# Kernel optimization log

Measured on AMD Instinct MI355X. Metric: run time of the kernel, lower is better.

## Reference

```python
import jax, jax.numpy as jnp
import numpy as np

E = 384          # embed_dim
NH = 12          # num_heads
HD = E // NH     # head_dim = 32
NC = 16          # num_clusters
SCALE = HD ** -0.5


def setup_inputs() -> dict:
    key = jax.random.key(0)
    ks = jax.random.split(key, 6)
    b, h, w = 8, 64, 64
    x = jax.random.normal(ks[0], (b, E, h, w), jnp.float32)
    qkv_w = jax.random.normal(ks[1], (3 * E, E), jnp.float32) * 0.02
    qkv_b = jnp.zeros((3 * E,), jnp.float32)
    lepe_w = jax.random.normal(ks[2], (E, 1, 5, 5), jnp.float32) * 0.02
    lepe_b = jnp.zeros((E,), jnp.float32)
    out_w = jax.random.normal(ks[3], (E, E), jnp.float32) * 0.02
    out_b = jnp.zeros((E,), jnp.float32)
    return dict(x=x, qkv_w=qkv_w, qkv_b=qkv_b, lepe_w=lepe_w,
                lepe_b=lepe_b, out_w=out_w, out_b=out_b)


def _gather_tokens(t, idx):
    # t: (b, n, l, d), idx: (b, n, l)
    return jnp.take_along_axis(t, idx[..., None], axis=2)


def reference(x, qkv_w, qkv_b, lepe_w, lepe_b, out_w, out_b):
    b, _, h, w = x.shape
    l = h * w
    lc = l // NC  # tokens per cluster

    # 1x1 conv qkv projection (channel order: [q heads | k heads | v heads])
    qkv = jnp.einsum('bchw,oc->bohw', x, qkv_w) + qkv_b[None, :, None, None]

    # lepe: 5x5 depthwise conv on the v channel slice
    v_img = qkv[:, 2 * E:]
    lepe = jax.lax.conv_general_dilated(
        v_img, lepe_w, (1, 1), ((2, 2), (2, 2)),
        feature_group_count=E,
        dimension_numbers=('NCHW', 'OIHW', 'NCHW')) + lepe_b[None, :, None, None]

    # 'b (m n d) h w -> m b n (h w) d'
    qkv = qkv.reshape(b, 3, NH, HD, l).transpose(1, 0, 2, 4, 3)  # (3,b,n,l,d)
    q, k, v = qkv[0], qkv[1], qkv[2]
    k = k * SCALE

    # cosine-similarity sort routing (sort_sim(k, k))
    cls = jnp.mean(k, axis=2, keepdims=True)                       # (b,n,1,d)
    cls = cls / jnp.maximum(jnp.linalg.norm(cls, axis=-1, keepdims=True), 1e-12)
    kn = k / jnp.maximum(jnp.linalg.norm(k, axis=-1, keepdims=True), 1e-12)
    cos = jnp.einsum('bnod,bnld->bnl', cls, kn)                    # (b,n,l)
    idx = jnp.argsort(cos, axis=-1)                                # (b,n,l)

    qs = _gather_tokens(q, idx).reshape(b, NH, NC, lc, HD)
    ks_ = _gather_tokens(k, idx).reshape(b, NH, NC, lc, HD)
    vs = _gather_tokens(v, idx).reshape(b, NH, NC, lc, HD)

    # blockwise (per-cluster) attention
    attn = jax.nn.softmax(jnp.einsum('bncld,bncmd->bnclm', qs, ks_), axis=-1)
    o = jnp.einsum('bnclm,bncmd->bncld', attn, vs).reshape(b, NH, l, HD)

    # restore original token order (inverse permutation)
    inv = jnp.argsort(idx, axis=-1)
    o = _gather_tokens(o, inv)

    # 'b n (h w) d -> b (n d) h w'
    o = o.transpose(0, 1, 3, 2).reshape(b, E, h, w)

    res = o + lepe
    return jnp.einsum('bchw,oc->bohw', res, out_w) + out_b[None, :, None, None]
```

## Files before the change

kernel.cpp:

```cpp
#include <hip/hip_runtime.h>
#include <math.h>

#define SCALE_F   0.17677669529663687f
#define SCALE_L2E 0.25505837072959003f

using bf16x8 = __attribute__((ext_vector_type(8))) __bf16;
using f32x2  = __attribute__((ext_vector_type(2))) float;
using f32x4  = __attribute__((ext_vector_type(4))) float;
using f32x16 = __attribute__((ext_vector_type(16))) float;
using uint2e = __attribute__((ext_vector_type(2))) unsigned int;

__device__ inline unsigned short f2bf(float x) {
    __bf16 h = (__bf16)x;
    return __builtin_bit_cast(unsigned short, h);
}
__device__ inline float bf2f(unsigned short u) {
    unsigned int x = ((unsigned int)u) << 16;
    return __builtin_bit_cast(float, x);
}
__device__ inline unsigned int packbf(float a, float b) {
    return (unsigned int)f2bf(a) | ((unsigned int)f2bf(b) << 16);
}
__device__ inline bf16x8 ldfrag(const unsigned short* p) {
    return __builtin_bit_cast(bf16x8, *reinterpret_cast<const uint4*>(p));
}

__global__ __launch_bounds__(512)
void gemm_k_kernel(const float* __restrict__ A, const float* __restrict__ Bmat,
                   const float* __restrict__ bias, float* __restrict__ CT)
{
    const int bm = blockIdx.x, bn = blockIdx.y, bz = blockIdx.z;
    const float* Bp = Bmat + (long)bz * 384 * 4096;
    float* Cp = CT + (long)bz * 4096 * 384;
    __shared__ float As[32][132];
    __shared__ float BsF[32 * 136];
    const int tid = threadIdx.x;
    const int tx = tid & 15, ty = tid >> 4;
    const int m0 = bm * 128, n0 = bn * 128;

    const int sr0 = tid >> 5,          sq0 = tid & 31;
    const int sr1 = (tid + 512) >> 5,  sq1 = (tid + 512) & 31;
    const int wB0 = sr0 * 136 + ((sq0 & 1) << 6) + ((sq0 >> 1) << 2);
    const int wB1 = sr1 * 136 + ((sq1 & 1) << 6) + ((sq1 >> 1) << 2);

    f32x2 acc2[4][4];
    #pragma unroll
    for (int i = 0; i < 4; ++i)
        #pragma unroll
        for (int p = 0; p < 4; ++p) acc2[i][p] = (f32x2){0.f, 0.f};

    float4 bPf0 = *reinterpret_cast<const float4*>(&Bp[(long)sr0 * 4096 + n0 + sq0 * 4]);
    float4 bPf1 = *reinterpret_cast<const float4*>(&Bp[(long)sr1 * 4096 + n0 + sq1 * 4]);

    for (int k0 = 0; k0 < 384; k0 += 32) {
        if (k0) __syncthreads();
        *reinterpret_cast<float4*>(&BsF[wB0]) = bPf0;
        *reinterpret_cast<float4*>(&BsF[wB1]) = bPf1;
        #pragma unroll
        for (int it = 0; it < 2; ++it) {
            int slot = tid + it * 512;
            int rA = slot >> 3, cA = slot & 7;
            float4 av = *reinterpret_cast<const float4*>(&A[(long)(384 + m0 + rA) * 384 + k0 + cA * 4]);
            As[cA * 4 + 0][rA] = av.x; As[cA * 4 + 1][rA] = av.y;
            As[cA * 4 + 2][rA] = av.z; As[cA * 4 + 3][rA] = av.w;
        }
        __syncthreads();
        if (k0 + 32 < 384) {
            bPf0 = *reinterpret_cast<const float4*>(&Bp[(long)(k0 + 32 + sr0) * 4096 + n0 + sq0 * 4]);
            bPf1 = *reinterpret_cast<const float4*>(&Bp[(long)(k0 + 32 + sr1) * 4096 + n0 + sq1 * 4]);
        }
        #pragma unroll
        for (int kk = 0; kk < 32; ++kk) {
            float a[4];
            *reinterpret_cast<float4*>(&a[0]) = *reinterpret_cast<const float4*>(&As[kk][ty * 4]);
            float4 blo = *reinterpret_cast<const float4*>(&BsF[kk * 136 + tx * 4]);
            float4 bhi = *reinterpret_cast<const float4*>(&BsF[kk * 136 + 64 + tx * 4]);
            f32x2 b2[4];
            b2[0] = (f32x2){blo.x, blo.y}; b2[1] = (f32x2){blo.z, blo.w};
            b2[2] = (f32x2){bhi.x, bhi.y}; b2[3] = (f32x2){bhi.z, bhi.w};
            #pragma unroll
            for (int i = 0; i < 4; ++i) {
                f32x2 a2 = (f32x2){a[i], a[i]};
                #pragma unroll
                for (int p = 0; p < 4; ++p)
                    acc2[i][p] = __builtin_elementwise_fma(a2, b2[p], acc2[i][p]);
            }
        }
    }

    float bv[4];
    #pragma unroll
    for (int i = 0; i < 4; ++i) bv[i] = bias[384 + m0 + ty * 4 + i];
    #pragma unroll
    for (int p = 0; p < 4; ++p)
        #pragma unroll
        for (int c = 0; c < 2; ++c) {
            int j = 2 * p + c;
            long tok = n0 + tx * 8 + j;
            float4 v = make_float4(acc2[0][p][c] + bv[0], acc2[1][p][c] + bv[1],
                                   acc2[2][p][c] + bv[2], acc2[3][p][c] + bv[3]);
            *reinterpret_cast<float4*>(Cp + tok * 384 + m0 + ty * 4) = v;
        }
}

template<bool SPLIT, int SM>
__global__ __launch_bounds__(256)
void mfma_nt_kernel(const unsigned short* __restrict__ Ah, const unsigned short* __restrict__ Al,
                    const unsigned short* __restrict__ Bh, const unsigned short* __restrict__ Bl,
                    const float* __restrict__ bias, void* __restrict__ Cout,
                    int K, int lda, int ldb,
                    long strideAb, long strideBb, long strideCb)
{
    extern __shared__ unsigned short smem[];
    unsigned short* As  = smem;
    unsigned short* Bs  = smem + 5120;
    unsigned short* Asl = smem + 10240;
    unsigned short* Bsl = smem + 15360;
    const int bm = blockIdx.x, bn = blockIdx.y, bz = blockIdx.z;
    const unsigned short* Ap = Ah + (long)bz * strideAb;
    const unsigned short* Bp = Bh + (long)bz * strideBb;
    const unsigned short* Alp = nullptr;
    const unsigned short* Blp = nullptr;
    if constexpr (SPLIT) {
        Alp = Al + (long)bz * strideAb;
        Blp = Bl + (long)bz * strideBb;
    }
    const int tid = threadIdx.x;
    const int lane = tid & 63, wid = tid >> 6;
    const int wr = wid >> 1, wc = wid & 1;
    const int l15 = lane & 15, l4 = lane >> 4;
    const int m0 = bm * 128, n0 = bn * 128;

    const f32x4 Z4 = {0.f, 0.f, 0.f, 0.f};
    f32x4 acc[4][4];
    #pragma unroll
    for (int i = 0; i < 4; ++i)
        #pragma unroll
        for (int j = 0; j < 4; ++j) acc[i][j] = Z4;

    for (int k0 = 0; k0 < K; k0 += 32) {
        if (k0) __syncthreads();
        #pragma unroll
        for (int it = 0; it < 2; ++it) {
            int slot = tid + it * 256;
            int r = slot >> 2, cq = slot & 3;
            *reinterpret_cast<uint4*>(&As[r * 40 + cq * 8]) =
                *reinterpret_cast<const uint4*>(&Ap[(long)(m0 + r) * lda + k0 + cq * 8]);
            *reinterpret_cast<uint4*>(&Bs[r * 40 + cq * 8]) =
                *reinterpret_cast<const uint4*>(&Bp[(long)(n0 + r) * ldb + k0 + cq * 8]);
            if constexpr (SPLIT) {
                *reinterpret_cast<uint4*>(&Asl[r * 40 + cq * 8]) =
                    *reinterpret_cast<const uint4*>(&Alp[(long)(m0 + r) * lda + k0 + cq * 8]);
                *reinterpret_cast<uint4*>(&Bsl[r * 40 + cq * 8]) =
                    *reinterpret_cast<const uint4*>(&Blp[(long)(n0 + r) * ldb + k0 + cq * 8]);
            }
        }
        __syncthreads();

        bf16x8 af[4], bg[4], afl[4], bgl[4];
        #pragma unroll
        for (int f = 0; f < 4; ++f) {
            af[f] = ldfrag(&As[(wr * 64 + f * 16 + l15) * 40 + l4 * 8]);
            bg[f] = ldfrag(&Bs[(wc * 64 + f * 16 + l15) * 40 + l4 * 8]);
        }
        if constexpr (SPLIT) {
            #pragma unroll
            for (int f = 0; f < 4; ++f) {
                afl[f] = ldfrag(&Asl[(wr * 64 + f * 16 + l15) * 40 + l4 * 8]);
                bgl[f] = ldfrag(&Bsl[(wc * 64 + f * 16 + l15) * 40 + l4 * 8]);
            }
        }
        #pragma unroll
        for (int fi = 0; fi < 4; ++fi)
            #pragma unroll
            for (int fj = 0; fj < 4; ++fj) {
                acc[fi][fj] = __builtin_amdgcn_mfma_f32_16x16x32_bf16(af[fi], bg[fj], acc[fi][fj], 0, 0, 0);
                if constexpr (SPLIT) {
                    acc[fi][fj] = __builtin_amdgcn_mfma_f32_16x16x32_bf16(af[fi], bgl[fj], acc[fi][fj], 0, 0, 0);
                    acc[fi][fj] = __builtin_amdgcn_mfma_f32_16x16x32_bf16(afl[fi], bg[fj], acc[fi][fj], 0, 0, 0);
                }
            }
    }

    if constexpr (SM == 0) {
        unsigned short* Cq = (unsigned short*)Cout + (long)bz * strideCb;
        #pragma unroll
        for (int fi = 0; fi < 4; ++fi)
            #pragma unroll
            for (int fj = 0; fj < 4; ++fj) {
                const int m = m0 + wr * 64 + fi * 16 + l4 * 4;
                const int t = n0 + wc * 64 + fj * 16 + l15;
                ushort4 h;
                h.x = f2bf(acc[fi][fj][0] + bias[m + 0]);
                h.y = f2bf(acc[fi][fj][1] + bias[m + 1]);
                h.z = f2bf(acc[fi][fj][2] + bias[m + 2]);
                h.w = f2bf(acc[fi][fj][3] + bias[m + 3]);
                *reinterpret_cast<ushort4*>(&Cq[(long)t * 768 + m]) = h;
            }
    } else {
        float* Cf = (float*)Cout + (long)bz * strideCb;
        #pragma unroll
        for (int fi = 0; fi < 4; ++fi)
            #pragma unroll
            for (int fj = 0; fj < 4; ++fj) {
                const int t = m0 + wr * 64 + fi * 16 + l4 * 4;
                const int m = n0 + wc * 64 + fj * 16 + l15;
                const float bv = bias[m];
                float4 v = make_float4(acc[fi][fj][0] + bv, acc[fi][fj][1] + bv,
                                       acc[fi][fj][2] + bv, acc[fi][fj][3] + bv);
                *reinterpret_cast<float4*>(&Cf[(long)m * 4096 + t]) = v;
            }
    }
}

__global__ __launch_bounds__(256)
void convert_w_kernel(const float* __restrict__ qkv_w, const float* __restrict__ qkv_b,
                      const float* __restrict__ out_w,
                      unsigned short* __restrict__ Wqv, float* __restrict__ qvb,
                      unsigned short* __restrict__ owh, unsigned short* __restrict__ owl)
{
    const int total = 294912 + 147456 + 768;
    for (int i = blockIdx.x * 256 + threadIdx.x; i < total; i += gridDim.x * 256) {
        if (i < 294912) {
            int m = i / 384, k = i - m * 384;
            int src = (m < 384) ? m : m + 384;
            Wqv[i] = f2bf(qkv_w[(long)src * 384 + k]);
        } else if (i < 294912 + 147456) {
            int o = i - 294912;
            float w = out_w[o];
            unsigned short h = f2bf(w);
            owh[o] = h;
            owl[o] = f2bf(w - bf2f(h));
        } else {
            int m = i - 294912 - 147456;
            qvb[m] = qkv_b[(m < 384) ? m : m + 384];
        }
    }
}

__global__ __launch_bounds__(256)
void transpose_x_kernel(const float* __restrict__ x, unsigned short* __restrict__ xbT)
{
    const int t0 = blockIdx.x * 64, c0 = blockIdx.y * 64, b = blockIdx.z;
    __shared__ float tl[64][65];
    const int tid = threadIdx.x;
    #pragma unroll
    for (int i = 0; i < 16; ++i) {
        int cr = (tid >> 6) + i * 4, tc = tid & 63;
        tl[cr][tc] = x[((long)b * 384 + c0 + cr) * 4096 + t0 + tc];
    }
    __syncthreads();
    #pragma unroll
    for (int i = 0; i < 8; ++i) {
        int tr = (tid >> 5) + i * 8, c2 = (tid & 31) * 2;
        unsigned int u = packbf(tl[c2][tr], tl[c2 + 1][tr]);
        *reinterpret_cast<unsigned int*>(&xbT[((long)b * 4096 + t0 + tr) * 384 + c0 + c2]) = u;
    }
}

__global__ __launch_bounds__(256)
void cls_kernel(const float* __restrict__ Kf32, float* __restrict__ clsg)
{
    const int bn = blockIdx.x;
    const int b = bn / 12, n = bn % 12;
    const float* kb = Kf32 + (long)b * 4096 * 384 + n * 32;
    __shared__ float part[256][33];
    const int tid = threadIdx.x;
    float acc[32];
    #pragma unroll
    for (int d = 0; d < 32; ++d) acc[d] = 0.f;
    for (int i = 0; i < 16; ++i) {
        long tok = tid + i * 256;
        const float* kr = kb + tok * 384;
        #pragma unroll
        for (int d = 0; d < 32; ++d) acc[d] += kr[d];
    }
    #pragma unroll
    for (int d = 0; d < 32; ++d) part[tid][d] = acc[d];
    __syncthreads();
    if (tid < 32) {
        double s = 0.0;
        for (int t = 0; t < 256; ++t) s += (double)part[t][tid];
        part[0][tid] = (float)s;
    }
    __syncthreads();
    if (tid == 0) {
        double nn = 0.0;
        for (int d = 0; d < 32; ++d) { double v = (double)part[0][d]; nn += v * v; }
        double inv = 1.0 / sqrt(nn > 1e-300 ? nn : 1e-300);
        for (int d = 0; d < 32; ++d) clsg[bn * 32 + d] = (float)((double)part[0][d] * inv);
    }
}

__global__ __launch_bounds__(256)
void cos_lepe_kernel(const float* __restrict__ Kf32, const float* __restrict__ clsg,
                     float* __restrict__ cosv,
                     const unsigned short* __restrict__ qvB, const float* __restrict__ w5,
                     const float* __restrict__ wb, unsigned short* __restrict__ lepeT)
{
    __shared__ float tile[12 * 68 * 16];
    const int bid = blockIdx.x;
    const int tid = threadIdx.x;

    if (bid < 1536) {
        const int ch0 = (bid % 24) * 16;
        const int y0 = ((bid / 24) % 8) * 8;
        const int b = bid / 192;
        const unsigned short* vb = qvB + (long)b * 4096 * 768 + 384 + ch0;
        unsigned short* dst = lepeT + (long)b * 4096 * 384 + ch0;

        for (int s = tid; s < 12 * 68 * 2; s += 256) {
            int pix = s >> 1, half = s & 1;
            int yy = pix / 68, xx = pix % 68;
            int gy = y0 + yy - 2, gx = xx - 2;
            float* tp = &tile[pix * 16 + half * 8];
            if (gy >= 0 && gy < 64 && gx >= 0 && gx < 64) {
                uint4 u = *reinterpret_cast<const uint4*>(vb + (long)(gy * 64 + gx) * 768 + half * 8);
                tp[0] = bf2f((unsigned short)(u.x & 0xFFFFu)); tp[1] = bf2f((unsigned short)(u.x >> 16));
                tp[2] = bf2f((unsigned short)(u.y & 0xFFFFu)); tp[3] = bf2f((unsigned short)(u.y >> 16));
                tp[4] = bf2f((unsigned short)(u.z & 0xFFFFu)); tp[5] = bf2f((unsigned short)(u.z >> 16));
                tp[6] = bf2f((unsigned short)(u.w & 0xFFFFu)); tp[7] = bf2f((unsigned short)(u.w >> 16));
            } else {
                #pragma unroll
                for (int j = 0; j < 8; ++j) tp[j] = 0.f;
            }
        }
        const int c = tid & 15, xo = tid >> 4;
        float f[25];
        #pragma unroll
        for (int j = 0; j < 25; ++j) f[j] = w5[(ch0 + c) * 25 + j];
        const float bv = wb[ch0 + c];
        __syncthreads();

        #pragma unroll
        for (int yy = 0; yy < 8; ++yy) {
            #pragma unroll
            for (int xq = 0; xq < 4; ++xq) {
                int x = xq * 16 + xo;
                float acc = bv;
                #pragma unroll
                for (int dy = 0; dy < 5; ++dy)
                    #pragma unroll
                    for (int dx = 0; dx < 5; ++dx)
                        acc += tile[((yy + dy) * 68 + (x + dx)) * 16 + c] * f[dy * 5 + dx];
                dst[(long)((y0 + yy) * 64 + x) * 384 + c] = f2bf(acc);
            }
        }
    } else {
        const int cb = bid - 1536;
        const int bn = cb % 96;
        const int b = bn / 12, n = bn % 12;
        const float* kb = Kf32 + (long)b * 4096 * 384 + n * 32;
        const int t0 = (cb / 96) * 512;
        float clsn[32];
        #pragma unroll
        for (int d = 0; d < 32; ++d) clsn[d] = clsg[bn * 32 + d];
        #pragma unroll
        for (int i = 0; i < 2; ++i) {
            long tok = t0 + tid + i * 256;
            const float* kr = kb + tok * 384;
            double dot = 0.0, nrm = 0.0;
            #pragma unroll
            for (int d = 0; d < 32; ++d) {
                float kv = kr[d];
                dot += (double)clsn[d] * (double)kv;
                nrm += (double)kv * (double)kv;
            }
            double cv = dot / sqrt(nrm > 1e-300 ? nrm : 1e-300);
            cosv[(long)bn * 4096 + tok] = (float)cv;
        }
    }
}

__global__ __launch_bounds__(1024)
void sort_kernel(const float* __restrict__ cosv, int* __restrict__ idxo)
{
    const int bn = blockIdx.x;
    __shared__ unsigned long long sk[4096];
    const int tid = threadIdx.x;
    for (int i = tid; i < 4096; i += 1024) {
        unsigned int u = __builtin_bit_cast(unsigned int, cosv[(long)bn * 4096 + i]);
        u = (u & 0x80000000u) ? ~u : (u | 0x80000000u);
        sk[i] = ((unsigned long long)u << 32) | (unsigned int)i;
    }
    __syncthreads();
    for (int size = 2; size <= 4096; size <<= 1) {
        for (int stride = size >> 1; stride >= 1; stride >>= 1) {
            #pragma unroll 2
            for (int i = tid; i < 2048; i += 1024) {
                int lo = (i << 1) - (i & (stride - 1));
                int hi = lo + stride;
                bool asc = ((lo & size) == 0);
                unsigned long long a = sk[lo], bq = sk[hi];
                if ((a > bq) == asc) { sk[lo] = bq; sk[hi] = a; }
            }
            __syncthreads();
        }
    }
    for (int i = tid; i < 4096; i += 1024)
        idxo[(long)bn * 4096 + i] = (int)(sk[i] & 0xFFFFFFFFu);
}

__global__ __launch_bounds__(256)
void attn_kernel(const float* __restrict__ Kf32, unsigned short* __restrict__ qvB,
                 const int* __restrict__ idxbuf, const unsigned short* __restrict__ lepeT)
{
    const int cc = blockIdx.x, n = blockIdx.y, b = blockIdx.z;
    const int* ip = idxbuf + ((long)(b * 12 + n)) * 4096 + cc * 256;

    __shared__ unsigned short KsL[256][36];
    __shared__ unsigned short VsT[32][260];
    __shared__ int tokLds[256];

    const int tid = threadIdx.x;
    const int w = tid >> 6;
    const int lane = tid & 63;
    const int lo5 = lane & 31;
    const int hi = lane >> 5;
    const int hi8 = hi * 8;

    const int tk0 = ip[tid];
    tokLds[tid] = tk0;
    const long tb = (long)b * 4096 + tk0;
    const unsigned short* qrow = qvB + tb * 768 + n * 32;
    const float* krow = Kf32 + tb * 384 + n * 32;

    unsigned int Pq[16];
    #pragma unroll
    for (int i = 0; i < 4; ++i) {
        uint4 qu = *reinterpret_cast<const uint4*>(qrow + i * 8);
        Pq[4 * i + 0] = qu.x; Pq[4 * i + 1] = qu.y;
        Pq[4 * i + 2] = qu.z; Pq[4 * i + 3] = qu.w;
    }
    #pragma unroll
    for (int dq = 0; dq < 8; ++dq) {
        float4 kv = *reinterpret_cast<const float4*>(krow + dq * 4);
        ushort4 kp;
        kp.x = f2bf(kv.x * SCALE_L2E); kp.y = f2bf(kv.y * SCALE_L2E);
        kp.z = f2bf(kv.z * SCALE_L2E); kp.w = f2bf(kv.w * SCALE_L2E);
        *reinterpret_cast<ushort4*>(&KsL[tid][dq * 4]) = kp;
    }
    {
        union { uint4 u[4]; unsigned short s[32]; } vv;
        const unsigned short* vrow = qrow + 384;
        #pragma unroll
        for (int i = 0; i < 4; ++i) vv.u[i] = *reinterpret_cast<const uint4*>(vrow + i * 8);
        #pragma unroll
        for (int j = 0; j < 32; ++j) VsT[j][tid] = vv.s[j];
    }

    bf16x8 qf00, qf01, qf10, qf11;
    {
        unsigned int w0[2][4], w1[2][4];
        #pragma unroll
        for (int ks = 0; ks < 2; ++ks)
            #pragma unroll
            for (int j = 0; j < 4; ++j) {
                uint2e r = __builtin_amdgcn_permlane32_swap(Pq[ks * 8 + j], Pq[ks * 8 + 4 + j], false, false);
                w0[ks][j] = r[0];
                w1[ks][j] = r[1];
            }
        qf00 = __builtin_bit_cast(bf16x8, make_uint4(w0[0][0], w0[0][1], w0[0][2], w0[0][3]));
        qf01 = __builtin_bit_cast(bf16x8, make_uint4(w0[1][0], w0[1][1], w0[1][2], w0[1][3]));
        qf10 = __builtin_bit_cast(bf16x8, make_uint4(w1[0][0], w1[0][1], w1[0][2], w1[0][3]));
        qf11 = __builtin_bit_cast(bf16x8, make_uint4(w1[1][0], w1[1][1], w1[1][2], w1[1][3]));
    }
    __syncthreads();

    const f32x16 Z16 = {0,0,0,0,0,0,0,0,0,0,0,0,0,0,0,0};
    f32x16 o0 = Z16, o1 = Z16;
    float lsum0 = 0.f, lsum1 = 0.f;

#define LDFRAG(ARR, ROW, OFF) ({ \
    const unsigned short* _p = &ARR[ROW][OFF]; \
    union { bf16x8 v; ushort4 h[2]; } _u; \
    _u.h[0] = *reinterpret_cast<const ushort4*>(_p); \
    _u.h[1] = *reinterpret_cast<const ushort4*>(_p + 4); \
    _u.v; })

#define EXP16(S, LS) { _Pragma("unroll") for (int r = 0; r < 16; ++r) { float _e = __builtin_exp2f(S[r]); S[r] = _e; LS += _e; } }

#define MKPB(S, H) ({ \
    unsigned int _x0 = packbf(S[(H) * 8 + 0], S[(H) * 8 + 1]); \
    unsigned int _x1 = packbf(S[(H) * 8 + 2], S[(H) * 8 + 3]); \
    unsigned int _x2 = packbf(S[(H) * 8 + 4], S[(H) * 8 + 5]); \
    unsigned int _x3 = packbf(S[(H) * 8 + 6], S[(H) * 8 + 7]); \
    uint2e _r02 = __builtin_amdgcn_permlane32_swap(_x0, _x2, false, false); \
    uint2e _r13 = __builtin_amdgcn_permlane32_swap(_x1, _x3, false, false); \
    __builtin_bit_cast(bf16x8, make_uint4(_r02[0], _r13[0], _r02[1], _r13[1])); })

    for (int ch = 0; ch < 4; ++ch) {
        const int rb = ch * 64;
        f32x16 s00 = Z16, s01 = Z16, s10 = Z16, s11 = Z16;
        bf16x8 ka;
        __builtin_amdgcn_s_setprio(1);
        ka = LDFRAG(KsL, rb + lo5, hi8);
        s00 = __builtin_amdgcn_mfma_f32_32x32x16_bf16(ka, qf00, s00, 0, 0, 0);
        s01 = __builtin_amdgcn_mfma_f32_32x32x16_bf16(ka, qf10, s01, 0, 0, 0);
        ka = LDFRAG(KsL, rb + lo5, 16 + hi8);
        s00 = __builtin_amdgcn_mfma_f32_32x32x16_bf16(ka, qf01, s00, 0, 0, 0);
        s01 = __builtin_amdgcn_mfma_f32_32x32x16_bf16(ka, qf11, s01, 0, 0, 0);
        ka = LDFRAG(KsL, rb + 32 + lo5, hi8);
        s10 = __builtin_amdgcn_mfma_f32_32x32x16_bf16(ka, qf00, s10, 0, 0, 0);
        s11 = __builtin_amdgcn_mfma_f32_32x32x16_bf16(ka, qf10, s11, 0, 0, 0);
        ka = LDFRAG(KsL, rb + 32 + lo5, 16 + hi8);
        s10 = __builtin_amdgcn_mfma_f32_32x32x16_bf16(ka, qf01, s10, 0, 0, 0);
        s11 = __builtin_amdgcn_mfma_f32_32x32x16_bf16(ka, qf11, s11, 0, 0, 0);
        __builtin_amdgcn_s_setprio(0);

        EXP16(s00, lsum0); EXP16(s01, lsum1);
        EXP16(s10, lsum0); EXP16(s11, lsum1);

        bf16x8 va, pb0, pb1;
        __builtin_amdgcn_s_setprio(1);
        va = LDFRAG(VsT, lo5, rb + 0 + hi8);
        pb0 = MKPB(s00, 0); pb1 = MKPB(s01, 0);
        o0 = __builtin_amdgcn_mfma_f32_32x32x16_bf16(va, pb0, o0, 0, 0, 0);
        o1 = __builtin_amdgcn_mfma_f32_32x32x16_bf16(va, pb1, o1, 0, 0, 0);
        va = LDFRAG(VsT, lo5, rb + 16 + hi8);
        pb0 = MKPB(s00, 1); pb1 = MKPB(s01, 1);
        o0 = __builtin_amdgcn_mfma_f32_32x32x16_bf16(va, pb0, o0, 0, 0, 0);
        o1 = __builtin_amdgcn_mfma_f32_32x32x16_bf16(va, pb1, o1, 0, 0, 0);
        va = LDFRAG(VsT, lo5, rb + 32 + hi8);
        pb0 = MKPB(s10, 0); pb1 = MKPB(s11, 0);
        o0 = __builtin_amdgcn_mfma_f32_32x32x16_bf16(va, pb0, o0, 0, 0, 0);
        o1 = __builtin_amdgcn_mfma_f32_32x32x16_bf16(va, pb1, o1, 0, 0, 0);
        va = LDFRAG(VsT, lo5, rb + 48 + hi8);
        pb0 = MKPB(s10, 1); pb1 = MKPB(s11, 1);
        o0 = __builtin_amdgcn_mfma_f32_32x32x16_bf16(va, pb0, o0, 0, 0, 0);
        o1 = __builtin_amdgcn_mfma_f32_32x32x16_bf16(va, pb1, o1, 0, 0, 0);
        __builtin_amdgcn_s_setprio(0);
    }

    const float lf0 = lsum0 + __shfl_xor(lsum0, 32);
    const float lf1 = lsum1 + __shfl_xor(lsum1, 32);
    const float li0 = 1.f / lf0, li1 = 1.f / lf1;

    #pragma unroll
    for (int qt = 0; qt < 2; ++qt) {
        const int qrix = w * 64 + qt * 32 + lo5;
        const int tk = tokLds[qrix];
        const long tb2 = (long)b * 4096 + tk;
        unsigned short* resrow = qvB + tb2 * 768;
        const unsigned short* lp = lepeT + tb2 * 384 + n * 32;
        const float li = qt ? li1 : li0;
        const f32x16& oo = qt ? o1 : o0;
        #pragma unroll
        for (int qd = 0; qd < 4; ++qd) {
            const int d0 = qd * 8 + hi * 4;
            ushort4 lv = *reinterpret_cast<const ushort4*>(lp + d0);
            float r0 = oo[qd * 4 + 0] * li + bf2f(lv.x);
            float r1 = oo[qd * 4 + 1] * li + bf2f(lv.y);
            float r2 = oo[qd * 4 + 2] * li + bf2f(lv.z);
            float r3 = oo[qd * 4 + 3] * li + bf2f(lv.w);
            unsigned short h0 = f2bf(r0), h1 = f2bf(r1), h2 = f2bf(r2), h3 = f2bf(r3);
            ushort4 hh = {h0, h1, h2, h3};
            ushort4 ll = {f2bf(r0 - bf2f(h0)), f2bf(r1 - bf2f(h1)),
                          f2bf(r2 - bf2f(h2)), f2bf(r3 - bf2f(h3))};
            *reinterpret_cast<ushort4*>(resrow + n * 32 + d0) = hh;
            *reinterpret_cast<ushort4*>(resrow + 384 + n * 32 + d0) = ll;
        }
    }
#undef LDFRAG
#undef EXP16
#undef MKPB
}

extern "C" void kernel_launch(void* const* d_in, const int* in_sizes, int n_in,
                              void* d_out, int out_size, void* d_ws, size_t ws_size,
                              hipStream_t stream)
{
    const float* x      = (const float*)d_in[0];
    const float* qkv_w  = (const float*)d_in[1];
    const float* qkv_b  = (const float*)d_in[2];
    const float* lepe_w = (const float*)d_in[3];
    const float* lepe_b = (const float*)d_in[4];
    const float* out_w  = (const float*)d_in[5];
    const float* out_b  = (const float*)d_in[6];
    float* out = (float*)d_out;

    char* ws = (char*)d_ws;
    float*          Kf32 = (float*)ws;
    unsigned short* qvB  = (unsigned short*)(ws + 50331648);
    float*          cosv = (float*)(ws + 100663296);
    int*            idx  = (int*)(ws + 102236160);
    unsigned short* Wqv  = (unsigned short*)(ws + 103809024);
    unsigned short* owh  = (unsigned short*)(ws + 104398848);
    unsigned short* owl  = (unsigned short*)(ws + 104693760);
    float*          qvb  = (float*)(ws + 104988672);
    float*          clsg = (float*)(ws + 104991744);

    unsigned short* xbT   = (unsigned short*)d_out;
    unsigned short* lepeT = (unsigned short*)d_out + 12582912;

    convert_w_kernel<<<1731, 256, 0, stream>>>(qkv_w, qkv_b, out_w, Wqv, qvb, owh, owl);
    transpose_x_kernel<<<dim3(64, 6, 8), 256, 0, stream>>>(x, xbT);
    gemm_k_kernel<<<dim3(3, 32, 8), 512, 0, stream>>>(qkv_w, x, qkv_b, Kf32);
    mfma_nt_kernel<false, 0><<<dim3(6, 32, 8), 256, 20480, stream>>>(
        Wqv, nullptr, xbT, nullptr, qvb, qvB,
        384, 384, 384, 0L, (long)4096 * 384, (long)4096 * 768);
    cls_kernel<<<96, 256, 0, stream>>>(Kf32, clsg);
    cos_lepe_kernel<<<2304, 256, 0, stream>>>(Kf32, clsg, cosv, qvB, lepe_w, lepe_b, lepeT);
    sort_kernel<<<96, 1024, 0, stream>>>(cosv, idx);
    attn_kernel<<<dim3(16, 12, 8), 256, 0, stream>>>(Kf32, qvB, idx, lepeT);
    mfma_nt_kernel<true, 1><<<dim3(32, 3, 8), 256, 40960, stream>>>(
        qvB, qvB + 384, owh, owl, out_b, out,
        384, 768, 384, (long)4096 * 768, 0L, (long)384 * 4096);
}
```

Before: 395.6 us.

## Merge weight-convert and x-transpose kernels; retile fp32 K GEMM to 256 threads

The weight conversion and x transpose/bf16 kernels are merged into one launch that splits work by block index, removing one kernel launch and letting the two jobs overlap. The fp32 K-projection GEMM moves from 512 threads with a 4x8 per-thread tile and packed f32x2 FMAs to 256 threads with an 8x8 per-thread tile. It also drops the register prefetch of the next B tile. The larger per-thread tile raises register use and gives up packed FMA and load/compute overlap in exchange for more reuse from shared-memory reads.

```diff
diff --git a/kernel.cpp b/kernel.cpp
--- a/kernel.cpp
+++ b/kernel.cpp
@@ -25,7 +25,7 @@
     return __builtin_bit_cast(bf16x8, *reinterpret_cast<const uint4*>(p));
 }
 
-__global__ __launch_bounds__(512)
+__global__ __launch_bounds__(256)
 void gemm_k_kernel(const float* __restrict__ A, const float* __restrict__ Bmat,
                    const float* __restrict__ bias, float* __restrict__ CT)
 {
@@ -38,69 +38,54 @@
     const int tx = tid & 15, ty = tid >> 4;
     const int m0 = bm * 128, n0 = bn * 128;
 
-    const int sr0 = tid >> 5,          sq0 = tid & 31;
-    const int sr1 = (tid + 512) >> 5,  sq1 = (tid + 512) & 31;
-    const int wB0 = sr0 * 136 + ((sq0 & 1) << 6) + ((sq0 >> 1) << 2);
-    const int wB1 = sr1 * 136 + ((sq1 & 1) << 6) + ((sq1 >> 1) << 2);
-
-    f32x2 acc2[4][4];
-    #pragma unroll
-    for (int i = 0; i < 4; ++i)
-        #pragma unroll
-        for (int p = 0; p < 4; ++p) acc2[i][p] = (f32x2){0.f, 0.f};
-
-    float4 bPf0 = *reinterpret_cast<const float4*>(&Bp[(long)sr0 * 4096 + n0 + sq0 * 4]);
-    float4 bPf1 = *reinterpret_cast<const float4*>(&Bp[(long)sr1 * 4096 + n0 + sq1 * 4]);
+    float acc[8][8];
+    #pragma unroll
+    for (int i = 0; i < 8; ++i)
+        #pragma unroll
+        for (int j = 0; j < 8; ++j) acc[i][j] = 0.f;
 
     for (int k0 = 0; k0 < 384; k0 += 32) {
         if (k0) __syncthreads();
-        *reinterpret_cast<float4*>(&BsF[wB0]) = bPf0;
-        *reinterpret_cast<float4*>(&BsF[wB1]) = bPf1;
-        #pragma unroll
-        for (int it = 0; it < 2; ++it) {
-            int slot = tid + it * 512;
+        #pragma unroll
+        for (int it = 0; it < 4; ++it) {
+            int slot = tid + it * 256;
             int rA = slot >> 3, cA = slot & 7;
             float4 av = *reinterpret_cast<const float4*>(&A[(long)(384 + m0 + rA) * 384 + k0 + cA * 4]);
             As[cA * 4 + 0][rA] = av.x; As[cA * 4 + 1][rA] = av.y;
             As[cA * 4 + 2][rA] = av.z; As[cA * 4 + 3][rA] = av.w;
+            int sr = slot >> 5, sq = slot & 31;
+            int wB = sr * 136 + ((sq & 1) << 6) + ((sq >> 1) << 2);
+            *reinterpret_cast<float4*>(&BsF[wB]) =
+                *reinterpret_cast<const float4*>(&Bp[(long)(k0 + sr) * 4096 + n0 + sq * 4]);
         }
         __syncthreads();
-        if (k0 + 32 < 384) {
-            bPf0 = *reinterpret_cast<const float4*>(&Bp[(long)(k0 + 32 + sr0) * 4096 + n0 + sq0 * 4]);
-            bPf1 = *reinterpret_cast<const float4*>(&Bp[(long)(k0 + 32 + sr1) * 4096 + n0 + sq1 * 4]);
-        }
         #pragma unroll
         for (int kk = 0; kk < 32; ++kk) {
-            float a[4];
-            *reinterpret_cast<float4*>(&a[0]) = *reinterpret_cast<const float4*>(&As[kk][ty * 4]);
-            float4 blo = *reinterpret_cast<const float4*>(&BsF[kk * 136 + tx * 4]);
-            float4 bhi = *reinterpret_cast<const float4*>(&BsF[kk * 136 + 64 + tx * 4]);
-            f32x2 b2[4];
-            b2[0] = (f32x2){blo.x, blo.y}; b2[1] = (f32x2){blo.z, blo.w};
-            b2[2] = (f32x2){bhi.x, bhi.y}; b2[3] = (f32x2){bhi.z, bhi.w};
-            #pragma unroll
-            for (int i = 0; i < 4; ++i) {
-                f32x2 a2 = (f32x2){a[i], a[i]};
+            float a[8], b[8];
+            *reinterpret_cast<float4*>(&a[0]) = *reinterpret_cast<const float4*>(&As[kk][ty * 8]);
+            *reinterpret_cast<float4*>(&a[4]) = *reinterpret_cast<const float4*>(&As[kk][ty * 8 + 4]);
+            *reinterpret_cast<float4*>(&b[0]) = *reinterpret_cast<const float4*>(&BsF[kk * 136 + tx * 4]);
+            *reinterpret_cast<float4*>(&b[4]) = *reinterpret_cast<const float4*>(&BsF[kk * 136 + 64 + tx * 4]);
+            #pragma unroll
+            for (int i = 0; i < 8; ++i)
                 #pragma unroll
-                for (int p = 0; p < 4; ++p)
-                    acc2[i][p] = __builtin_elementwise_fma(a2, b2[p], acc2[i][p]);
-            }
-        }
-    }
-
-    float bv[4];
-    #pragma unroll
-    for (int i = 0; i < 4; ++i) bv[i] = bias[384 + m0 + ty * 4 + i];
-    #pragma unroll
-    for (int p = 0; p < 4; ++p)
-        #pragma unroll
-        for (int c = 0; c < 2; ++c) {
-            int j = 2 * p + c;
-            long tok = n0 + tx * 8 + j;
-            float4 v = make_float4(acc2[0][p][c] + bv[0], acc2[1][p][c] + bv[1],
-                                   acc2[2][p][c] + bv[2], acc2[3][p][c] + bv[3]);
-            *reinterpret_cast<float4*>(Cp + tok * 384 + m0 + ty * 4) = v;
-        }
+                for (int j = 0; j < 8; ++j)
+                    acc[i][j] += a[i] * b[j];
+        }
+    }
+
+    float bv[8];
+    #pragma unroll
+    for (int i = 0; i < 8; ++i) bv[i] = bias[384 + m0 + ty * 8 + i];
+    #pragma unroll
+    for (int j = 0; j < 8; ++j) {
+        long tok = n0 + tx * 8 + j;
+        float* ptr = Cp + tok * 384 + m0 + ty * 8;
+        float4 lo = make_float4(acc[0][j] + bv[0], acc[1][j] + bv[1], acc[2][j] + bv[2], acc[3][j] + bv[3]);
+        float4 hi = make_float4(acc[4][j] + bv[4], acc[5][j] + bv[5], acc[6][j] + bv[6], acc[7][j] + bv[7]);
+        *reinterpret_cast<float4*>(ptr) = lo;
+        *reinterpret_cast<float4*>(ptr + 4) = hi;
+    }
 }
 
 template<bool SPLIT, int SM>
@@ -214,47 +199,47 @@
 }
 
 __global__ __launch_bounds__(256)
-void convert_w_kernel(const float* __restrict__ qkv_w, const float* __restrict__ qkv_b,
-                      const float* __restrict__ out_w,
-                      unsigned short* __restrict__ Wqv, float* __restrict__ qvb,
-                      unsigned short* __restrict__ owh, unsigned short* __restrict__ owl)
-{
-    const int total = 294912 + 147456 + 768;
-    for (int i = blockIdx.x * 256 + threadIdx.x; i < total; i += gridDim.x * 256) {
-        if (i < 294912) {
-            int m = i / 384, k = i - m * 384;
-            int src = (m < 384) ? m : m + 384;
-            Wqv[i] = f2bf(qkv_w[(long)src * 384 + k]);
-        } else if (i < 294912 + 147456) {
-            int o = i - 294912;
-            float w = out_w[o];
-            unsigned short h = f2bf(w);
-            owh[o] = h;
-            owl[o] = f2bf(w - bf2f(h));
-        } else {
-            int m = i - 294912 - 147456;
-            qvb[m] = qkv_b[(m < 384) ? m : m + 384];
-        }
-    }
-}
-
-__global__ __launch_bounds__(256)
-void transpose_x_kernel(const float* __restrict__ x, unsigned short* __restrict__ xbT)
-{
-    const int t0 = blockIdx.x * 64, c0 = blockIdx.y * 64, b = blockIdx.z;
+void prep_kernel(const float* __restrict__ x, unsigned short* __restrict__ xbT,
+                 const float* __restrict__ qkv_w, const float* __restrict__ qkv_b,
+                 const float* __restrict__ out_w,
+                 unsigned short* __restrict__ Wqv, float* __restrict__ qvb,
+                 unsigned short* __restrict__ owh, unsigned short* __restrict__ owl)
+{
     __shared__ float tl[64][65];
-    const int tid = threadIdx.x;
-    #pragma unroll
-    for (int i = 0; i < 16; ++i) {
-        int cr = (tid >> 6) + i * 4, tc = tid & 63;
-        tl[cr][tc] = x[((long)b * 384 + c0 + cr) * 4096 + t0 + tc];
-    }
-    __syncthreads();
-    #pragma unroll
-    for (int i = 0; i < 8; ++i) {
-        int tr = (tid >> 5) + i * 8, c2 = (tid & 31) * 2;
-        unsigned int u = packbf(tl[c2][tr], tl[c2 + 1][tr]);
-        *reinterpret_cast<unsigned int*>(&xbT[((long)b * 4096 + t0 + tr) * 384 + c0 + c2]) = u;
+    const int bid = blockIdx.x;
+    const int tid = threadIdx.x;
+    if (bid < 3072) {
+        const int t0 = (bid % 64) * 64, c0 = ((bid / 64) % 6) * 64, b = bid / 384;
+        #pragma unroll
+        for (int i = 0; i < 16; ++i) {
+            int cr = (tid >> 6) + i * 4, tc = tid & 63;
+            tl[cr][tc] = x[((long)b * 384 + c0 + cr) * 4096 + t0 + tc];
+        }
+        __syncthreads();
+        #pragma unroll
+        for (int i = 0; i < 8; ++i) {
+            int tr = (tid >> 5) + i * 8, c2 = (tid & 31) * 2;
+            unsigned int u = packbf(tl[c2][tr], tl[c2 + 1][tr]);
+            *reinterpret_cast<unsigned int*>(&xbT[((long)b * 4096 + t0 + tr) * 384 + c0 + c2]) = u;
+        }
+    } else {
+        const int total = 294912 + 147456 + 768;
+        for (int i = (bid - 3072) * 256 + tid; i < total; i += 1731 * 256) {
+            if (i < 294912) {
+                int m = i / 384, k = i - m * 384;
+                int src = (m < 384) ? m : m + 384;
+                Wqv[i] = f2bf(qkv_w[(long)src * 384 + k]);
+            } else if (i < 294912 + 147456) {
+                int o = i - 294912;
+                float w = out_w[o];
+                unsigned short h = f2bf(w);
+                owh[o] = h;
+                owl[o] = f2bf(w - bf2f(h));
+            } else {
+                int m = i - 294912 - 147456;
+                qvb[m] = qkv_b[(m < 384) ? m : m + 384];
+            }
+        }
     }
 }
 
@@ -593,9 +578,8 @@
     unsigned short* xbT   = (unsigned short*)d_out;
     unsigned short* lepeT = (unsigned short*)d_out + 12582912;
 
-    convert_w_kernel<<<1731, 256, 0, stream>>>(qkv_w, qkv_b, out_w, Wqv, qvb, owh, owl);
-    transpose_x_kernel<<<dim3(64, 6, 8), 256, 0, stream>>>(x, xbT);
-    gemm_k_kernel<<<dim3(3, 32, 8), 512, 0, stream>>>(qkv_w, x, qkv_b, Kf32);
+    prep_kernel<<<4803, 256, 0, stream>>>(x, xbT, qkv_w, qkv_b, out_w, Wqv, qvb, owh, owl);
+    gemm_k_kernel<<<dim3(3, 32, 8), 256, 0, stream>>>(qkv_w, x, qkv_b, Kf32);
     mfma_nt_kernel<false, 0><<<dim3(6, 32, 8), 256, 20480, stream>>>(
         Wqv, nullptr, xbT, nullptr, qvb, qvB,
         384, 384, 384, 0L, (long)4096 * 384, (long)4096 * 768);
```

Result: no change. 394.3 us (-0.3%).
